# Kernel optimization log

Hardware: AMD Instinct MI355X
Metric: run time of the kernel (lower is better)

Reference implementation:

```python
import jax, jax.numpy as jnp
import numpy as np

N, M, D = 50000, 16, 128

def setup_inputs() -> dict:
    key = jax.random.key(0)
    k1, k2, k3, k4 = jax.random.split(key, 4)
    x = jax.random.normal(k1, (N, D), dtype=jnp.float32)
    # 1-based neighbor indices in [1, N] (module does x[x_nb - 1])
    x_nb = jax.random.randint(k2, (N, M), 1, N + 1)
    # xavier_normal-ish scale for W [d,d] and a [1,2d]
    W = jax.random.normal(k3, (D, D), dtype=jnp.float32) * np.float32(np.sqrt(2.0 / (D + D)))
    a = jax.random.normal(k4, (1, 2 * D), dtype=jnp.float32) * np.float32(np.sqrt(2.0 / (2 * D + 1)))
    return {"x": x, "x_nb": x_nb, "W": W, "a": a}

def reference(x, x_nb, W, a):
    # x: [n,d], x_nb: [n,m] 1-based, W: [d,d], a: [1,2d]
    n, d = x.shape
    idx = x_nb - 1                      # [n,m] 0-based
    z = x[idx]                          # [n,m,d] gathered neighbor feats
    h = x @ W.T                         # [n,d] = W(x); note W(z) = h[idx]
    a_self = a[0, :d]                   # split of concat-linear: a([h_i, h_j]) = h_i.a1 + h_j.a2
    a_nb = a[0, d:]
    s_self = h @ a_self                 # [n]
    s_nb = (h @ a_nb)[idx]              # [n,m]
    e = jax.nn.leaky_relu(s_self[:, None] + s_nb, negative_slope=0.01)  # [n,m]
    alpha = jax.nn.softmax(e, axis=1)   # softmax over neighbors
    u = jnp.sum(alpha[..., None] * z, axis=1)  # [n,d]
    return jax.nn.elu(u)
```

## Files before the change

### kernel.cpp

```cpp
#include <hip/hip_runtime.h>
#include <math.h>
#include <string.h>

#define NN 50000
#define MM 16
#define DD 128

__global__ __launch_bounds__(512) void compute_v_kernel(
        const float* __restrict__ W, const float* __restrict__ a,
        float* __restrict__ v) {
    __shared__ float svs[4][DD];
    __shared__ float svn[4][DD];
    int j  = threadIdx.x & 127;
    int kc = threadIdx.x >> 7;
    float vs = 0.f, vn = 0.f;
#pragma unroll 4
    for (int k = kc * 32; k < kc * 32 + 32; ++k) {
        float w = W[k * DD + j];
        vs += w * a[k];
        vn += w * a[DD + k];
    }
    svs[kc][j] = vs;
    svn[kc][j] = vn;
    __syncthreads();
    if (kc == 0) {
        v[j]      = svs[0][j] + svs[1][j] + svs[2][j] + svs[3][j];
        v[DD + j] = svn[0][j] + svn[1][j] + svn[2][j] + svn[3][j];
    }
}

__global__ __launch_bounds__(256) void prep_kernel(
        const float* __restrict__ x, const float* __restrict__ v,
        float* __restrict__ sself, float2* __restrict__ nbdat,
        unsigned short* __restrict__ xq) {
    int node = (blockIdx.x * blockDim.x + threadIdx.x) >> 6;
    int lane = threadIdx.x & 63;
    if (node >= NN) return;

    double xr = __builtin_nontemporal_load(
        reinterpret_cast<const double*>(x + (size_t)node * DD + 2 * lane));
    float2 xv; memcpy(&xv, &xr, 8);

    const float2 vs = *reinterpret_cast<const float2*>(v + 2 * lane);
    const float2 vn = *reinterpret_cast<const float2*>(v + DD + 2 * lane);

    float am = fmaxf(fabsf(xv.x), fabsf(xv.y));
    for (int off = 32; off >= 1; off >>= 1) am = fmaxf(am, __shfl_xor(am, off, 64));
    float sc  = am / 127.f;
    float inv = am > 0.f ? 127.f / am : 0.f;

    int q0 = (int)rintf(xv.x * inv);
    int q1 = (int)rintf(xv.y * inv);
    xq[(size_t)node * (DD / 2) + lane] =
        (unsigned short)((q0 & 0xff) | ((q1 & 0xff) << 8));

    float ps = xv.x * vs.x + xv.y * vs.y;
    float pn = xv.x * vn.x + xv.y * vn.y;
    for (int off = 32; off >= 1; off >>= 1) {
        ps += __shfl_down(ps, off, 64);
        pn += __shfl_down(pn, off, 64);
    }
    if (lane == 0) {
        sself[node] = ps;
        nbdat[node] = make_float2(pn, sc);
    }
}

__global__ __launch_bounds__(256) void agg_q8_kernel(
        const unsigned short* __restrict__ xq, const int* __restrict__ x_nb,
        const float* __restrict__ sself, const float2* __restrict__ nbdat,
        float* __restrict__ out) {
    int node = (blockIdx.x * blockDim.x + threadIdx.x) >> 6;
    int lane = threadIdx.x & 63;
    if (node >= NN) return;
    int o = lane & 15;
    int g = lane >> 4;

    int idxv = x_nb[(size_t)node * MM + o] - 1;
    float2 nd = nbdat[idxv];
    float sv = sself[node] + nd.x;
    float ev = sv > 0.f ? sv : 0.01f * sv;

    float mx = ev;
    for (int off = 8; off >= 1; off >>= 1) mx = fmaxf(mx, __shfl_xor(mx, off, 64));
    float ex = __expf(ev - mx);
    float sum = ex;
    for (int off = 8; off >= 1; off >>= 1) sum += __shfl_xor(sum, off, 64);
    float coef = (ex / sum) * nd.y;

    const uint2* xq8 = reinterpret_cast<const uint2*>(xq);
    float u0 = 0.f, u1 = 0.f, u2 = 0.f, u3 = 0.f;
    float u4 = 0.f, u5 = 0.f, u6 = 0.f, u7 = 0.f;
#pragma unroll
    for (int t = 0; t < 4; ++t) {
        int m    = 4 * t + g;
        int id   = __shfl(idxv, m, 64);
        float cf = __shfl(coef, m, 64);
        uint2 p  = xq8[(size_t)id * (DD / 8) + o];
        u0 += cf * (float)(signed char)(p.x);
        u1 += cf * (float)(signed char)(p.x >> 8);
        u2 += cf * (float)(signed char)(p.x >> 16);
        u3 += cf * (float)(signed char)(p.x >> 24);
        u4 += cf * (float)(signed char)(p.y);
        u5 += cf * (float)(signed char)(p.y >> 8);
        u6 += cf * (float)(signed char)(p.y >> 16);
        u7 += cf * (float)(signed char)(p.y >> 24);
    }
#pragma unroll
    for (int off = 16; off <= 32; off <<= 1) {
        u0 += __shfl_xor(u0, off, 64);
        u1 += __shfl_xor(u1, off, 64);
        u2 += __shfl_xor(u2, off, 64);
        u3 += __shfl_xor(u3, off, 64);
        u4 += __shfl_xor(u4, off, 64);
        u5 += __shfl_xor(u5, off, 64);
        u6 += __shfl_xor(u6, off, 64);
        u7 += __shfl_xor(u7, off, 64);
    }
    float a0, a1;
    if      (g == 0) { a0 = u0; a1 = u1; }
    else if (g == 1) { a0 = u2; a1 = u3; }
    else if (g == 2) { a0 = u4; a1 = u5; }
    else             { a0 = u6; a1 = u7; }
    a0 = a0 > 0.f ? a0 : __expf(a0) - 1.f;
    a1 = a1 > 0.f ? a1 : __expf(a1) - 1.f;
    float2 w; w.x = a0; w.y = a1;
    double dw; memcpy(&dw, &w, 8);
    __builtin_nontemporal_store(dw,
        reinterpret_cast<double*>(out + (size_t)node * DD + 8 * o + 2 * g));
}

__global__ __launch_bounds__(256) void scores_kernel(
        const float* __restrict__ x, const float* __restrict__ v,
        float* __restrict__ sself, float* __restrict__ snb) {
    int wave = (blockIdx.x * blockDim.x + threadIdx.x) >> 6;
    int lane = threadIdx.x & 63;
    if (wave >= NN) return;
    const float2 xv = *reinterpret_cast<const float2*>(x + (size_t)wave * DD + 2 * lane);
    const float2 vs = *reinterpret_cast<const float2*>(v + 2 * lane);
    const float2 vn = *reinterpret_cast<const float2*>(v + DD + 2 * lane);
    float ps = xv.x * vs.x + xv.y * vs.y;
    float pn = xv.x * vn.x + xv.y * vn.y;
    for (int off = 32; off >= 1; off >>= 1) {
        ps += __shfl_down(ps, off, 64);
        pn += __shfl_down(pn, off, 64);
    }
    if (lane == 0) { sself[wave] = ps; snb[wave] = pn; }
}

__global__ __launch_bounds__(256) void agg_kernel(
        const float* __restrict__ x, const int* __restrict__ x_nb,
        const float* __restrict__ sself, const float* __restrict__ snb,
        float* __restrict__ out) {
    int node = (blockIdx.x * blockDim.x + threadIdx.x) >> 6;
    int lane = threadIdx.x & 63;
    if (node >= NN) return;
    int m = lane & 15;
    int idxv = x_nb[(size_t)node * MM + m] - 1;
    float sv = sself[node] + snb[idxv];
    float ev = sv > 0.f ? sv : 0.01f * sv;
    float mx = ev;
    for (int off = 8; off >= 1; off >>= 1) mx = fmaxf(mx, __shfl_xor(mx, off, 64));
    float ex = __expf(ev - mx);
    float sum = ex;
    for (int off = 8; off >= 1; off >>= 1) sum += __shfl_xor(sum, off, 64);
    float alpha = ex / sum;
    float ux = 0.f, uy = 0.f;
#pragma unroll
    for (int mm = 0; mm < MM; ++mm) {
        int id   = __shfl(idxv, mm, 64);
        float al = __shfl(alpha, mm, 64);
        const float2 xv = *reinterpret_cast<const float2*>(x + (size_t)id * DD + 2 * lane);
        ux += al * xv.x;
        uy += al * xv.y;
    }
    ux = ux > 0.f ? ux : __expf(ux) - 1.f;
    uy = uy > 0.f ? uy : __expf(uy) - 1.f;
    float2 oo; oo.x = ux; oo.y = uy;
    *reinterpret_cast<float2*>(out + (size_t)node * DD + 2 * lane) = oo;
}

extern "C" void kernel_launch(void* const* d_in, const int* in_sizes, int n_in,
                              void* d_out, int out_size, void* d_ws, size_t ws_size,
                              hipStream_t stream) {
    const float* x    = (const float*)d_in[0];
    const int*   x_nb = (const int*)d_in[1];
    const float* W    = (const float*)d_in[2];
    const float* a    = (const float*)d_in[3];
    float* out = (float*)d_out;

    float*  v     = (float*)d_ws;
    float*  sself = v + 256;
    float2* nbdat = (float2*)(sself + NN);
    unsigned short* xq = (unsigned short*)((char*)nbdat + (size_t)NN * 8);

    const size_t need_q8 = (size_t)256 * 4 + (size_t)NN * 4 + (size_t)NN * 8
                         + (size_t)NN * (DD / 2) * 2;

    compute_v_kernel<<<1, 512, 0, stream>>>(W, a, v);

    int blocks = (NN * 64 + 255) / 256;
    if (ws_size >= need_q8) {
        prep_kernel<<<blocks, 256, 0, stream>>>(x, v, sself, nbdat, xq);
        agg_q8_kernel<<<blocks, 256, 0, stream>>>(xq, x_nb, sself, nbdat, out);
    } else {
        float* snb = (float*)nbdat;
        scores_kernel<<<blocks, 256, 0, stream>>>(x, v, sself, snb);
        agg_kernel<<<blocks, 256, 0, stream>>>(x, x_nb, sself, snb, out);
    }
}
```

Measured before the change: 48.48 us.

## Remap int8 aggregation to four nodes per wave with batched neighbor loads

The quantized aggregation kernel now gives each 16-lane group its own node, so one wave handles four nodes instead of one. Each lane issues all 16 neighbor-row loads up front before computing the softmax, which keeps more memory requests in flight. Because each lane now owns 8 contiguous output features, the cross-group shuffle reduction and the select logic are gone, and results are written with two float4 stores. The prep kernel also switches from a nontemporal load of x to a plain load. The cost is more registers per lane for the 16 preloaded rows, which may lower occupancy.

New measurement: 44.82 us. 7.5% less time.

```diff
diff --git a/kernel.cpp b/kernel.cpp
--- a/kernel.cpp
+++ b/kernel.cpp
@@ -1,6 +1,5 @@
 #include <hip/hip_runtime.h>
 #include <math.h>
-#include <string.h>
 
 #define NN 50000
 #define MM 16
@@ -36,11 +35,7 @@
     int node = (blockIdx.x * blockDim.x + threadIdx.x) >> 6;
     int lane = threadIdx.x & 63;
     if (node >= NN) return;
-
-    double xr = __builtin_nontemporal_load(
-        reinterpret_cast<const double*>(x + (size_t)node * DD + 2 * lane));
-    float2 xv; memcpy(&xv, &xr, 8);
-
+    const float2 xv = *reinterpret_cast<const float2*>(x + (size_t)node * DD + 2 * lane);
     const float2 vs = *reinterpret_cast<const float2*>(v + 2 * lane);
     const float2 vn = *reinterpret_cast<const float2*>(v + DD + 2 * lane);
 
@@ -70,33 +65,46 @@
         const unsigned short* __restrict__ xq, const int* __restrict__ x_nb,
         const float* __restrict__ sself, const float2* __restrict__ nbdat,
         float* __restrict__ out) {
-    int node = (blockIdx.x * blockDim.x + threadIdx.x) >> 6;
-    int lane = threadIdx.x & 63;
+    int wave = (blockIdx.x * blockDim.x + threadIdx.x) >> 6;
+    int lane = threadIdx.x & 63;
+    int grp  = lane >> 4;
+    int o    = lane & 15;
+    int node = wave * 4 + grp;
     if (node >= NN) return;
-    int o = lane & 15;
-    int g = lane >> 4;
-
-    int idxv = x_nb[(size_t)node * MM + o] - 1;
+
+    int idxv = x_nb[(size_t)wave * 64 + lane] - 1;
+
     float2 nd = nbdat[idxv];
-    float sv = sself[node] + nd.x;
+    float s0  = sself[node];
+
+    int ids[16];
+#pragma unroll
+    for (int m = 0; m < 16; ++m)
+        ids[m] = __shfl(idxv, grp * 16 + m, 64);
+
+    const uint2* xq8 = reinterpret_cast<const uint2*>(xq);
+    uint2 r[16];
+#pragma unroll
+    for (int m = 0; m < 16; ++m)
+        r[m] = xq8[(size_t)ids[m] * (DD / 8) + o];
+
+    float sv = s0 + nd.x;
     float ev = sv > 0.f ? sv : 0.01f * sv;
-
     float mx = ev;
+#pragma unroll
     for (int off = 8; off >= 1; off >>= 1) mx = fmaxf(mx, __shfl_xor(mx, off, 64));
     float ex = __expf(ev - mx);
     float sum = ex;
+#pragma unroll
     for (int off = 8; off >= 1; off >>= 1) sum += __shfl_xor(sum, off, 64);
     float coef = (ex / sum) * nd.y;
 
-    const uint2* xq8 = reinterpret_cast<const uint2*>(xq);
     float u0 = 0.f, u1 = 0.f, u2 = 0.f, u3 = 0.f;
     float u4 = 0.f, u5 = 0.f, u6 = 0.f, u7 = 0.f;
 #pragma unroll
-    for (int t = 0; t < 4; ++t) {
-        int m    = 4 * t + g;
-        int id   = __shfl(idxv, m, 64);
-        float cf = __shfl(coef, m, 64);
-        uint2 p  = xq8[(size_t)id * (DD / 8) + o];
+    for (int m = 0; m < 16; ++m) {
+        float cf = __shfl(coef, grp * 16 + m, 64);
+        uint2 p  = r[m];
         u0 += cf * (float)(signed char)(p.x);
         u1 += cf * (float)(signed char)(p.x >> 8);
         u2 += cf * (float)(signed char)(p.x >> 16);
@@ -106,28 +114,17 @@
         u6 += cf * (float)(signed char)(p.y >> 16);
         u7 += cf * (float)(signed char)(p.y >> 24);
     }
-#pragma unroll
-    for (int off = 16; off <= 32; off <<= 1) {
-        u0 += __shfl_xor(u0, off, 64);
-        u1 += __shfl_xor(u1, off, 64);
-        u2 += __shfl_xor(u2, off, 64);
-        u3 += __shfl_xor(u3, off, 64);
-        u4 += __shfl_xor(u4, off, 64);
-        u5 += __shfl_xor(u5, off, 64);
-        u6 += __shfl_xor(u6, off, 64);
-        u7 += __shfl_xor(u7, off, 64);
-    }
-    float a0, a1;
-    if      (g == 0) { a0 = u0; a1 = u1; }
-    else if (g == 1) { a0 = u2; a1 = u3; }
-    else if (g == 2) { a0 = u4; a1 = u5; }
-    else             { a0 = u6; a1 = u7; }
-    a0 = a0 > 0.f ? a0 : __expf(a0) - 1.f;
-    a1 = a1 > 0.f ? a1 : __expf(a1) - 1.f;
-    float2 w; w.x = a0; w.y = a1;
-    double dw; memcpy(&dw, &w, 8);
-    __builtin_nontemporal_store(dw,
-        reinterpret_cast<double*>(out + (size_t)node * DD + 8 * o + 2 * g));
+    u0 = u0 > 0.f ? u0 : __expf(u0) - 1.f;
+    u1 = u1 > 0.f ? u1 : __expf(u1) - 1.f;
+    u2 = u2 > 0.f ? u2 : __expf(u2) - 1.f;
+    u3 = u3 > 0.f ? u3 : __expf(u3) - 1.f;
+    u4 = u4 > 0.f ? u4 : __expf(u4) - 1.f;
+    u5 = u5 > 0.f ? u5 : __expf(u5) - 1.f;
+    u6 = u6 > 0.f ? u6 : __expf(u6) - 1.f;
+    u7 = u7 > 0.f ? u7 : __expf(u7) - 1.f;
+    float4* op = reinterpret_cast<float4*>(out + (size_t)node * DD + 8 * o);
+    op[0] = make_float4(u0, u1, u2, u3);
+    op[1] = make_float4(u4, u5, u6, u7);
 }
 
 __global__ __launch_bounds__(256) void scores_kernel(
@@ -199,12 +196,15 @@
 
     compute_v_kernel<<<1, 512, 0, stream>>>(W, a, v);
 
-    int blocks = (NN * 64 + 255) / 256;
     if (ws_size >= need_q8) {
-        prep_kernel<<<blocks, 256, 0, stream>>>(x, v, sself, nbdat, xq);
-        agg_q8_kernel<<<blocks, 256, 0, stream>>>(xq, x_nb, sself, nbdat, out);
+        int blocks_prep = (NN * 64 + 255) / 256;
+        prep_kernel<<<blocks_prep, 256, 0, stream>>>(x, v, sself, nbdat, xq);
+        int waves_agg  = (NN + 3) / 4;
+        int blocks_agg = (waves_agg * 64 + 255) / 256;
+        agg_q8_kernel<<<blocks_agg, 256, 0, stream>>>(xq, x_nb, sself, nbdat, out);
     } else {
         float* snb = (float*)nbdat;
+        int blocks = (NN * 64 + 255) / 256;
         scores_kernel<<<blocks, 256, 0, stream>>>(x, v, sself, snb);
         agg_kernel<<<blocks, 256, 0, stream>>>(x, x_nb, sself, snb, out);
     }
```
